# Performance work log

Hardware: AMD Instinct MI355X
Metric: run time of the kernel (lower is better)

## Reference

```python
import jax, jax.numpy as jnp
import numpy as np

F_DIM = 128
RBF_DIM = 20
N_NODES = 10000
N_EDGES = 200000
CUTOFF = 5


def setup_inputs() -> dict:
    key = jax.random.key(0)
    ks = jax.random.split(key, 12)
    s = jax.random.normal(ks[0], (N_NODES, F_DIM), jnp.float32)
    vec = jax.random.normal(ks[1], (N_NODES, 3, F_DIM), jnp.float32)
    edge_indexes = jax.random.randint(ks[2], (2, N_EDGES), 0, N_NODES, jnp.int32)
    edge_vector = jax.random.normal(ks[3], (N_EDGES, 3), jnp.float32)
    # distances in (0.5, 5.0) so fcut is nontrivial and no divide-by-zero
    edge_distance = jax.random.uniform(ks[4], (N_EDGES,), jnp.float32) * 4.5 + 0.5
    edge_rbf = jax.random.normal(ks[5], (N_EDGES, RBF_DIM), jnp.float32)
    # params: linear_s = Linear(F,F) -> SiLU -> Linear(F,3F); linear_rbf = Linear(RBF,3F)
    Ws1 = jax.random.normal(ks[6], (F_DIM, F_DIM), jnp.float32) / np.sqrt(F_DIM)
    bs1 = jnp.zeros((F_DIM,), jnp.float32)
    Ws2 = jax.random.normal(ks[7], (3 * F_DIM, F_DIM), jnp.float32) / np.sqrt(F_DIM)
    bs2 = jnp.zeros((3 * F_DIM,), jnp.float32)
    Wrbf = jax.random.normal(ks[8], (3 * F_DIM, RBF_DIM), jnp.float32) / np.sqrt(RBF_DIM)
    brbf = jnp.zeros((3 * F_DIM,), jnp.float32)
    return {
        "s": s, "vec": vec, "edge_vector": edge_vector,
        "edge_distance": edge_distance, "edge_rbf": edge_rbf,
        "Ws1": Ws1, "bs1": bs1, "Ws2": Ws2, "bs2": bs2,
        "Wrbf": Wrbf, "brbf": brbf,
        "edge_indexes": edge_indexes, "cutoff_dist": CUTOFF,
    }


def reference(s, vec, edge_vector, edge_distance, edge_rbf,
              Ws1, bs1, Ws2, bs2, Wrbf, brbf,
              edge_indexes, cutoff_dist):
    num_atoms, nf = s.shape
    dst_recv = edge_indexes[0]   # index_add target (message receivers)
    src_send = edge_indexes[1]   # gather source (message senders)

    S = s[src_send]              # [E, F]
    Vec = vec[src_send]          # [E, 3, F]

    # linear_s: Linear -> SiLU -> Linear
    h = jax.nn.silu(S @ Ws1.T + bs1)          # [E, F]
    phi = h @ Ws2.T + bs2                      # [E, 3F]

    rbf_lin = edge_rbf @ Wrbf.T + brbf         # [E, 3F]
    # cosine cutoff: 0.5*(cos(pi*d/rc)+1) for d < rc else 0
    rc = jnp.asarray(cutoff_dist, edge_distance.dtype)
    fcut = 0.5 * (jnp.cos(jnp.pi * edge_distance / rc) + 1.0)
    fcut = jnp.where(edge_distance < rc, fcut, 0.0)

    W = rbf_lin * fcut[:, None]
    vec_Ws, vec_Wvv, vec_Wvs = jnp.split(phi * W, 3, axis=-1)  # each [E, F]

    ds = jnp.zeros((num_atoms, nf), s.dtype).at[dst_recv].add(vec_Ws)

    vec_n = edge_vector / edge_distance[:, None]               # [E, 3]
    dVec = vec_Wvv[:, None, :] * Vec + vec_n[:, :, None] * vec_Wvs[:, None, :]  # [E,3,F]
    dvec = jnp.zeros((num_atoms, 3, nf), s.dtype).at[dst_recv].add(dVec)

    return ds, dvec
```

## Files before the change

kernel.cpp:

```cpp
#include <hip/hip_runtime.h>
#include <hip/hip_bf16.h>

typedef __attribute__((ext_vector_type(8))) short short8;
typedef __attribute__((ext_vector_type(4))) float floatx4;
typedef _Float16 half2_t __attribute__((ext_vector_type(2)));

#define CAP 64

__device__ __forceinline__ unsigned short f2bf(float x) {
    unsigned u = __float_as_uint(x);
    unsigned r = u + 0x7fffu + ((u >> 16) & 1u);
    return (unsigned short)(r >> 16);
}
__device__ __forceinline__ float bf2f(unsigned short h) {
    return __uint_as_float(((unsigned)h) << 16);
}
__device__ __forceinline__ unsigned short f2h(float x) {
    _Float16 h = (_Float16)x;
    return __builtin_bit_cast(unsigned short, h);
}
__device__ __forceinline__ short8 cvt8(float4 x0, float4 x1) {
    short8 v;
    v[0] = (short)f2bf(x0.x); v[1] = (short)f2bf(x0.y);
    v[2] = (short)f2bf(x0.z); v[3] = (short)f2bf(x0.w);
    v[4] = (short)f2bf(x1.x); v[5] = (short)f2bf(x1.y);
    v[6] = (short)f2bf(x1.z); v[7] = (short)f2bf(x1.w);
    return v;
}
__device__ __forceinline__ float FD(unsigned int a, unsigned int b, float c) {
#if __has_builtin(__builtin_amdgcn_fdot2)
    return __builtin_amdgcn_fdot2(__builtin_bit_cast(half2_t, a),
                                  __builtin_bit_cast(half2_t, b), c, false);
#else
    half2_t ha = __builtin_bit_cast(half2_t, a);
    half2_t hb = __builtin_bit_cast(half2_t, b);
    return c + (float)ha[0] * (float)hb[0] + (float)ha[1] * (float)hb[1];
#endif
}
__device__ __forceinline__ float decode_rc(const void* cutoff_raw) {
    float fv = ((const float*)cutoff_raw)[0];
    int   iv = ((const int*)cutoff_raw)[0];
    if (fv > 0.099f && fv < 1.0e6f) return fv;
    if (iv > 0 && iv < 1000000) return (float)iv;
    double dv = ((const double*)cutoff_raw)[0];
    if (dv > 0.099 && dv < 1.0e6) return (float)dv;
    return (float)(((const long long*)cutoff_raw)[0]);
}

#define LN 136
__global__ __launch_bounds__(256, 4)
void produce_kernel(const float* __restrict__ s,
                    const float* __restrict__ vec,
                    const float* __restrict__ Ws1,
                    const float* __restrict__ bs1,
                    const float* __restrict__ Ws2,
                    const float* __restrict__ bs2,
                    const float* __restrict__ Wrbf,
                    const float* __restrict__ edge_rbf,
                    const int* __restrict__ eidx,
                    const float* __restrict__ edge_vec,
                    const float* __restrict__ edge_dist,
                    const void* __restrict__ cutoff_raw,
                    unsigned short* __restrict__ P6,
                    unsigned short* __restrict__ wrbf_h,
                    unsigned short* __restrict__ rbf_h,
                    int* __restrict__ cnt,
                    unsigned int* __restrict__ rec,
                    int Nn, int RB, int E,
                    int nb_node, int nb_sc,
                    int ng_vec, int ng_wh, int ng_rh)
{
    const int bid = (int)blockIdx.x;
    const int tid = threadIdx.x;

    __shared__ unsigned short S_bf[16][LN];
    __shared__ unsigned short H_bf[16][LN];

    if (bid < nb_node) {
        const int wv   = tid >> 6;
        const int lane = tid & 63;
        const int l15  = lane & 15;
        const int qq   = lane >> 4;
        const int base = bid * 16;

        {
            int row = tid >> 4;
            int col = (tid & 15) * 8;
            int node = base + row;
            short8 v;
            if (node < Nn) {
                const float4* sp4 = (const float4*)(s + (size_t)node * 128 + col);
                v = cvt8(sp4[0], sp4[1]);
            } else {
                #pragma unroll
                for (int k = 0; k < 8; ++k) v[k] = 0;
            }
            *((short8*)&S_bf[row][col]) = v;
        }
        __syncthreads();

        {
            short8 a[4];
            #pragma unroll
            for (int ks = 0; ks < 4; ++ks)
                a[ks] = *((const short8*)&S_bf[l15][ks * 32 + qq * 8]);
            floatx4 acc1[2];
            #pragma unroll
            for (int t = 0; t < 2; ++t) acc1[t] = (floatx4){0.f, 0.f, 0.f, 0.f};
            #pragma unroll
            for (int ks = 0; ks < 4; ++ks) {
                #pragma unroll
                for (int t = 0; t < 2; ++t) {
                    int nj = wv * 2 + t;
                    const float* wr = Ws1 + (size_t)(nj * 16 + l15) * 128 + ks * 32 + qq * 8;
                    short8 b = cvt8(((const float4*)wr)[0], ((const float4*)wr)[1]);
                    acc1[t] = __builtin_amdgcn_mfma_f32_16x16x32_bf16(a[ks], b, acc1[t], 0, 0, 0);
                }
            }
            #pragma unroll
            for (int t = 0; t < 2; ++t) {
                int nj = wv * 2 + t;
                float b1 = bs1[nj * 16 + l15];
                #pragma unroll
                for (int r = 0; r < 4; ++r) {
                    float x = acc1[t][r] + b1;
                    float h = x / (1.0f + __expf(-x));
                    H_bf[qq * 4 + r][nj * 16 + l15] = f2bf(h);
                }
            }
        }
        __syncthreads();

        {
            short8 a[4];
            #pragma unroll
            for (int ks = 0; ks < 4; ++ks)
                a[ks] = *((const short8*)&H_bf[l15][ks * 32 + qq * 8]);
            #pragma unroll
            for (int t6 = 0; t6 < 6; ++t6) {
                int t = wv * 6 + t6;
                int n = t * 16 + l15;
                floatx4 acc = (floatx4){0.f, 0.f, 0.f, 0.f};
                #pragma unroll
                for (int ks = 0; ks < 4; ++ks) {
                    const float* wr = Ws2 + (size_t)n * 128 + ks * 32 + qq * 8;
                    short8 b = cvt8(((const float4*)wr)[0], ((const float4*)wr)[1]);
                    acc = __builtin_amdgcn_mfma_f32_16x16x32_bf16(a[ks], b, acc, 0, 0, 0);
                }
                float b2 = bs2[n];
                #pragma unroll
                for (int r = 0; r < 4; ++r) {
                    int node = base + qq * 4 + r;
                    if (node < Nn)
                        P6[(size_t)node * 768 + n] = f2bf(acc[r] + b2);
                }
            }
        }
    } else if (bid < nb_node + nb_sc) {
        int i = (bid - nb_node) * 256 + tid;
        if (i >= E) return;
        float rc = decode_rc(cutoff_raw);
        int d = eidx[i];
        int slot = atomicAdd(&cnt[d], 1);
        if (slot >= CAP) return;
        float dist = edge_dist[i];
        float fc = 0.0f;
        if (dist < rc) fc = 0.5f * (cosf(3.14159265358979323846f * dist / rc) + 1.0f);
        float inv = 1.0f / dist;
        unsigned int* rp = rec + ((size_t)(d * CAP + slot) << 3);
        ((uint4*)rp)[0] = make_uint4((unsigned)eidx[E + i], (unsigned)i, 0u, 0u);
        ((uint4*)rp)[1] = make_uint4(__float_as_uint(edge_vec[i * 3 + 0] * inv),
                                     __float_as_uint(edge_vec[i * 3 + 1] * inv),
                                     __float_as_uint(edge_vec[i * 3 + 2] * inv),
                                     __float_as_uint(fc));
    } else {
        int total = ng_vec + ng_wh + ng_rh;
        int nbc = (int)gridDim.x - nb_node - nb_sc;
        int stride = nbc * 256;
        for (int g = (bid - nb_node - nb_sc) * 256 + tid; g < total; g += stride) {
            if (g < ng_vec) {
                int node = g / 48;
                int r = (g - node * 48) * 8;
                const float4* sp = (const float4*)(vec + (size_t)node * 384 + r);
                *(short8*)(P6 + (size_t)node * 768 + 384 + r) = cvt8(sp[0], sp[1]);
            } else if (g < ng_vec + ng_wh) {
                int gg = g - ng_vec;
                int n = gg >> 2, k0 = (gg & 3) * 8;
                short8 v;
                #pragma unroll
                for (int t = 0; t < 8; ++t) {
                    int k = k0 + t;
                    v[t] = (k < RB) ? (short)f2h(Wrbf[(size_t)n * RB + k]) : (short)0;
                }
                *(short8*)(wrbf_h + n * 32 + k0) = v;
            } else {
                int gg = g - ng_vec - ng_wh;
                int e = gg / 3, k0 = (gg - e * 3) * 8;
                short8 v;
                #pragma unroll
                for (int t = 0; t < 8; ++t) {
                    int k = k0 + t;
                    v[t] = (k < RB) ? (short)f2h(edge_rbf[(size_t)e * RB + k]) : (short)0;
                }
                *(short8*)(rbf_h + (size_t)e * 24 + k0) = v;
            }
        }
    }
}

__global__ __launch_bounds__(256, 6)
void edge_kernel(const unsigned short* __restrict__ P6,
                 const unsigned short* __restrict__ wrbf_h,
                 const float* __restrict__ brbf,
                 const int* __restrict__ cnt,
                 const unsigned int* __restrict__ rec,
                 const unsigned short* __restrict__ rbf_h,
                 float* __restrict__ out_ds,
                 float* __restrict__ out_dvec,
                 int Nn)
{
    const int tid  = threadIdx.x;
    const int w    = tid >> 6;
    const int lane = tid & 63;
    const int node = __builtin_amdgcn_readfirstlane((int)blockIdx.x * 2 + (w >> 1));
    const int c    = (w & 1) * 64 + lane;
    if (node >= Nn) return;

    const unsigned short* wp0 = wrbf_h + ((size_t)c << 5);
    const unsigned short* wp1 = wrbf_h + ((size_t)(128 + c) << 5);
    const unsigned short* wp2 = wrbf_h + ((size_t)(256 + c) << 5);
    uint4 w0a = *(const uint4*)wp0;
    uint4 w0b = *(const uint4*)(wp0 + 8);
    uint2 w0c = *(const uint2*)(wp0 + 16);
    uint4 w1a = *(const uint4*)wp1;
    uint4 w1b = *(const uint4*)(wp1 + 8);
    uint2 w1c = *(const uint2*)(wp1 + 16);
    uint4 w2a = *(const uint4*)wp2;
    uint4 w2b = *(const uint4*)(wp2 + 8);
    uint2 w2c = *(const uint2*)(wp2 + 16);
    float b0 = brbf[c];
    float b1 = brbf[128 + c];
    float b2 = brbf[256 + c];
    asm volatile("" : "+v"(w0a.x), "+v"(w0a.y), "+v"(w0a.z), "+v"(w0a.w),
                      "+v"(w0b.x), "+v"(w0b.y), "+v"(w0b.z), "+v"(w0b.w),
                      "+v"(w0c.x), "+v"(w0c.y));
    asm volatile("" : "+v"(w1a.x), "+v"(w1a.y), "+v"(w1a.z), "+v"(w1a.w),
                      "+v"(w1b.x), "+v"(w1b.y), "+v"(w1b.z), "+v"(w1b.w),
                      "+v"(w1c.x), "+v"(w1c.y));
    asm volatile("" : "+v"(w2a.x), "+v"(w2a.y), "+v"(w2a.z), "+v"(w2a.w),
                      "+v"(w2b.x), "+v"(w2b.y), "+v"(w2b.z), "+v"(w2b.w),
                      "+v"(w2c.x), "+v"(w2c.y),
                      "+v"(b0), "+v"(b1), "+v"(b2));

    const int deg = min(cnt[node], CAP);
    const size_t bb = (size_t)node * CAP;

    float as = 0.f, a0 = 0.f, a1 = 0.f, a2 = 0.f;

    if (deg > 0) {
        const uint4* rp = (const uint4*)(rec + (bb << 3));
        uint4 sm = rp[0], mq = rp[1];
        const unsigned short* rr = rbf_h + (size_t)(int)sm.y * 24;
        uint4 Ra = *(const uint4*)rr;
        uint4 Rb = *(const uint4*)(rr + 8);
        uint2 Rc = *(const uint2*)(rr + 16);

        for (int sl = 0; sl < deg; ++sl) {
            const unsigned short* pr = P6 + (size_t)(int)sm.x * 768;
            unsigned short u0 = pr[c];
            unsigned short u1 = pr[128 + c];
            unsigned short u2 = pr[256 + c];
            unsigned short u3 = pr[384 + c];
            unsigned short u4 = pr[512 + c];
            unsigned short u5 = pr[640 + c];

            int np = (sl + 1 < deg) ? (sl + 1) : sl;
            uint4 smn = rp[2 * np], mqn = rp[2 * np + 1];
            const unsigned short* rrn = rbf_h + (size_t)(int)smn.y * 24;
            uint4 Ran = *(const uint4*)rrn;
            uint4 Rbn = *(const uint4*)(rrn + 8);
            uint2 Rcn = *(const uint2*)(rrn + 16);

            float d0 = b0, d1 = b1, d2 = b2;
            d0 = FD(Ra.x, w0a.x, d0); d1 = FD(Ra.x, w1a.x, d1); d2 = FD(Ra.x, w2a.x, d2);
            d0 = FD(Ra.y, w0a.y, d0); d1 = FD(Ra.y, w1a.y, d1); d2 = FD(Ra.y, w2a.y, d2);
            d0 = FD(Ra.z, w0a.z, d0); d1 = FD(Ra.z, w1a.z, d1); d2 = FD(Ra.z, w2a.z, d2);
            d0 = FD(Ra.w, w0a.w, d0); d1 = FD(Ra.w, w1a.w, d1); d2 = FD(Ra.w, w2a.w, d2);
            d0 = FD(Rb.x, w0b.x, d0); d1 = FD(Rb.x, w1b.x, d1); d2 = FD(Rb.x, w2b.x, d2);
            d0 = FD(Rb.y, w0b.y, d0); d1 = FD(Rb.y, w1b.y, d1); d2 = FD(Rb.y, w2b.y, d2);
            d0 = FD(Rb.z, w0b.z, d0); d1 = FD(Rb.z, w1b.z, d1); d2 = FD(Rb.z, w2b.z, d2);
            d0 = FD(Rb.w, w0b.w, d0); d1 = FD(Rb.w, w1b.w, d1); d2 = FD(Rb.w, w2b.w, d2);
            d0 = FD(Rc.x, w0c.x, d0); d1 = FD(Rc.x, w1c.x, d1); d2 = FD(Rc.x, w2c.x, d2);
            d0 = FD(Rc.y, w0c.y, d0); d1 = FD(Rc.y, w1c.y, d1); d2 = FD(Rc.y, w2c.y, d2);

            float ps = bf2f(u0), pv = bf2f(u1), px = bf2f(u2);
            float v0 = bf2f(u3), v1 = bf2f(u4), v2 = bf2f(u5);

            float fc = __uint_as_float(mq.w);
            float W0 = d0 * fc, W1 = d1 * fc, W2 = d2 * fc;
            as = fmaf(ps, W0, as);
            float mv = pv * W1;
            float mx = px * W2;
            a0 = fmaf(mv, v0, fmaf(mx, __uint_as_float(mq.x), a0));
            a1 = fmaf(mv, v1, fmaf(mx, __uint_as_float(mq.y), a1));
            a2 = fmaf(mv, v2, fmaf(mx, __uint_as_float(mq.z), a2));

            sm = smn; mq = mqn; Ra = Ran; Rb = Rbn; Rc = Rcn;
        }
    }

    __builtin_nontemporal_store(as, out_ds + (size_t)node * 128 + c);
    float* od = out_dvec + (size_t)node * 384;
    __builtin_nontemporal_store(a0, od + c);
    __builtin_nontemporal_store(a1, od + 128 + c);
    __builtin_nontemporal_store(a2, od + 256 + c);
}

extern "C" void kernel_launch(void* const* d_in, const int* in_sizes, int n_in,
                              void* d_out, int out_size, void* d_ws, size_t ws_size,
                              hipStream_t stream) {
    const float* s        = (const float*)d_in[0];
    const float* vec      = (const float*)d_in[1];
    const float* edge_vec = (const float*)d_in[2];
    const float* edge_dst = (const float*)d_in[3];
    const float* edge_rbf = (const float*)d_in[4];
    const float* Ws1      = (const float*)d_in[5];
    const float* bs1      = (const float*)d_in[6];
    const float* Ws2      = (const float*)d_in[7];
    const float* bs2      = (const float*)d_in[8];
    const float* Wrbf     = (const float*)d_in[9];
    const float* brbf     = (const float*)d_in[10];
    const int*   eidx     = (const int*)d_in[11];
    const void*  cutoff   = d_in[12];

    const int F  = 128;
    const int Nn = in_sizes[0] / F;
    const int E  = in_sizes[3];
    const int RB = in_sizes[4] / E;
    const int F3 = 3 * F;

    unsigned int*   rec     = (unsigned int*)d_ws;
    unsigned short* P6      = (unsigned short*)(rec + (size_t)Nn * CAP * 8);
    unsigned short* rbf_h   = P6 + (size_t)Nn * 768;
    unsigned short* wrbf_h  = rbf_h + (size_t)E * 24;
    int* cnt                = (int*)(wrbf_h + F3 * 32);

    int ng_vec = (Nn * F3) >> 3;
    int ng_wh  = (F3 * 32) >> 3;
    int ng_rh  = (E * 24) >> 3;

    hipMemsetAsync(cnt, 0, (size_t)Nn * sizeof(int), stream);

    int nb_node = (Nn + 15) / 16;
    int nb_sc   = (E + 255) / 256;
    long long total_g = (long long)ng_vec + ng_wh + ng_rh;
    int nb_cast = (int)((total_g + 255) / 256);

    produce_kernel<<<nb_node + nb_sc + nb_cast, 256, 0, stream>>>(
        s, vec, Ws1, bs1, Ws2, bs2, Wrbf, edge_rbf,
        eidx, edge_vec, edge_dst, cutoff,
        P6, wrbf_h, rbf_h, cnt, rec,
        Nn, RB, E, nb_node, nb_sc,
        ng_vec, ng_wh, ng_rh);

    float* out_ds   = (float*)d_out;
    float* out_dvec = out_ds + (size_t)Nn * F;

    edge_kernel<<<(Nn + 1) / 2, 256, 0, stream>>>(P6, wrbf_h, brbf,
                                                  cnt, rec, rbf_h,
                                                  out_ds, out_dvec, Nn);
}
```

Before: 194.5 us.

## Pack fp16 RBF features directly into per-receiver edge records

The scatter phase now reads each edge's 20 RBF values, converts them to fp16 and stores them inside the per-receiver bucket record, which grows from 32 to 64 bytes. The separate rbf_h cast pass and the edge kernel's indirect gather through the edge id are removed, so the edge loop reads one contiguous record per neighbour. Scatter blocks are also moved to the front of the grid so they get scheduled first. The cost is a larger record buffer and more scattered write traffic in the scatter phase.

```diff
diff --git a/kernel.cpp b/kernel.cpp
--- a/kernel.cpp
+++ b/kernel.cpp
@@ -63,12 +63,11 @@
                     const void* __restrict__ cutoff_raw,
                     unsigned short* __restrict__ P6,
                     unsigned short* __restrict__ wrbf_h,
-                    unsigned short* __restrict__ rbf_h,
                     int* __restrict__ cnt,
                     unsigned int* __restrict__ rec,
                     int Nn, int RB, int E,
-                    int nb_node, int nb_sc,
-                    int ng_vec, int ng_wh, int ng_rh)
+                    int nb_sc, int nb_node,
+                    int ng_vec, int ng_wh)
 {
     const int bid = (int)blockIdx.x;
     const int tid = threadIdx.x;
@@ -76,12 +75,41 @@
     __shared__ unsigned short S_bf[16][LN];
     __shared__ unsigned short H_bf[16][LN];
 
-    if (bid < nb_node) {
+    if (bid < nb_sc) {
+        int i = bid * 256 + tid;
+        if (i >= E) return;
+        float rc = decode_rc(cutoff_raw);
+        int d = eidx[i];
+        int slot = atomicAdd(&cnt[d], 1);
+        if (slot >= CAP) return;
+        float dist = edge_dist[i];
+        float fc = 0.0f;
+        if (dist < rc) fc = 0.5f * (cosf(3.14159265358979323846f * dist / rc) + 1.0f);
+        float inv = 1.0f / dist;
+
+        float x[20];
+        const float* rr = edge_rbf + (size_t)i * RB;
+        #pragma unroll
+        for (int k = 0; k < 20; ++k) x[k] = (k < RB) ? rr[k] : 0.0f;
+        unsigned pk[10];
+        #pragma unroll
+        for (int k = 0; k < 10; ++k)
+            pk[k] = (unsigned)f2h(x[2 * k]) | ((unsigned)f2h(x[2 * k + 1]) << 16);
+
+        unsigned int* rp = rec + ((size_t)(d * CAP + slot) << 4);
+        ((uint4*)rp)[0] = make_uint4((unsigned)eidx[E + i], __float_as_uint(fc),
+                                     __float_as_uint(edge_vec[i * 3 + 0] * inv),
+                                     __float_as_uint(edge_vec[i * 3 + 1] * inv));
+        ((uint4*)rp)[1] = make_uint4(__float_as_uint(edge_vec[i * 3 + 2] * inv),
+                                     pk[0], pk[1], pk[2]);
+        ((uint4*)rp)[2] = make_uint4(pk[3], pk[4], pk[5], pk[6]);
+        ((uint4*)rp)[3] = make_uint4(pk[7], pk[8], pk[9], 0u);
+    } else if (bid < nb_sc + nb_node) {
         const int wv   = tid >> 6;
         const int lane = tid & 63;
         const int l15  = lane & 15;
         const int qq   = lane >> 4;
-        const int base = bid * 16;
+        const int base = (bid - nb_sc) * 16;
 
         {
             int row = tid >> 4;
@@ -156,34 +184,17 @@
                 }
             }
         }
-    } else if (bid < nb_node + nb_sc) {
-        int i = (bid - nb_node) * 256 + tid;
-        if (i >= E) return;
-        float rc = decode_rc(cutoff_raw);
-        int d = eidx[i];
-        int slot = atomicAdd(&cnt[d], 1);
-        if (slot >= CAP) return;
-        float dist = edge_dist[i];
-        float fc = 0.0f;
-        if (dist < rc) fc = 0.5f * (cosf(3.14159265358979323846f * dist / rc) + 1.0f);
-        float inv = 1.0f / dist;
-        unsigned int* rp = rec + ((size_t)(d * CAP + slot) << 3);
-        ((uint4*)rp)[0] = make_uint4((unsigned)eidx[E + i], (unsigned)i, 0u, 0u);
-        ((uint4*)rp)[1] = make_uint4(__float_as_uint(edge_vec[i * 3 + 0] * inv),
-                                     __float_as_uint(edge_vec[i * 3 + 1] * inv),
-                                     __float_as_uint(edge_vec[i * 3 + 2] * inv),
-                                     __float_as_uint(fc));
     } else {
-        int total = ng_vec + ng_wh + ng_rh;
-        int nbc = (int)gridDim.x - nb_node - nb_sc;
+        int total = ng_vec + ng_wh;
+        int nbc = (int)gridDim.x - nb_sc - nb_node;
         int stride = nbc * 256;
-        for (int g = (bid - nb_node - nb_sc) * 256 + tid; g < total; g += stride) {
+        for (int g = (bid - nb_sc - nb_node) * 256 + tid; g < total; g += stride) {
             if (g < ng_vec) {
                 int node = g / 48;
                 int r = (g - node * 48) * 8;
                 const float4* sp = (const float4*)(vec + (size_t)node * 384 + r);
                 *(short8*)(P6 + (size_t)node * 768 + 384 + r) = cvt8(sp[0], sp[1]);
-            } else if (g < ng_vec + ng_wh) {
+            } else {
                 int gg = g - ng_vec;
                 int n = gg >> 2, k0 = (gg & 3) * 8;
                 short8 v;
@@ -193,16 +204,6 @@
                     v[t] = (k < RB) ? (short)f2h(Wrbf[(size_t)n * RB + k]) : (short)0;
                 }
                 *(short8*)(wrbf_h + n * 32 + k0) = v;
-            } else {
-                int gg = g - ng_vec - ng_wh;
-                int e = gg / 3, k0 = (gg - e * 3) * 8;
-                short8 v;
-                #pragma unroll
-                for (int t = 0; t < 8; ++t) {
-                    int k = k0 + t;
-                    v[t] = (k < RB) ? (short)f2h(edge_rbf[(size_t)e * RB + k]) : (short)0;
-                }
-                *(short8*)(rbf_h + (size_t)e * 24 + k0) = v;
             }
         }
     }
@@ -214,7 +215,6 @@
                  const float* __restrict__ brbf,
                  const int* __restrict__ cnt,
                  const unsigned int* __restrict__ rec,
-                 const unsigned short* __restrict__ rbf_h,
                  float* __restrict__ out_ds,
                  float* __restrict__ out_dvec,
                  int Nn)
@@ -258,15 +258,11 @@
     float as = 0.f, a0 = 0.f, a1 = 0.f, a2 = 0.f;
 
     if (deg > 0) {
-        const uint4* rp = (const uint4*)(rec + (bb << 3));
-        uint4 sm = rp[0], mq = rp[1];
-        const unsigned short* rr = rbf_h + (size_t)(int)sm.y * 24;
-        uint4 Ra = *(const uint4*)rr;
-        uint4 Rb = *(const uint4*)(rr + 8);
-        uint2 Rc = *(const uint2*)(rr + 16);
+        const uint4* rp = (const uint4*)(rec + (bb << 4));
+        uint4 q0 = rp[0], q1 = rp[1], q2 = rp[2], q3 = rp[3];
 
         for (int sl = 0; sl < deg; ++sl) {
-            const unsigned short* pr = P6 + (size_t)(int)sm.x * 768;
+            const unsigned short* pr = P6 + (size_t)(int)q0.x * 768;
             unsigned short u0 = pr[c];
             unsigned short u1 = pr[128 + c];
             unsigned short u2 = pr[256 + c];
@@ -275,37 +271,34 @@
             unsigned short u5 = pr[640 + c];
 
             int np = (sl + 1 < deg) ? (sl + 1) : sl;
-            uint4 smn = rp[2 * np], mqn = rp[2 * np + 1];
-            const unsigned short* rrn = rbf_h + (size_t)(int)smn.y * 24;
-            uint4 Ran = *(const uint4*)rrn;
-            uint4 Rbn = *(const uint4*)(rrn + 8);
-            uint2 Rcn = *(const uint2*)(rrn + 16);
+            uint4 n0 = rp[4 * np], n1 = rp[4 * np + 1];
+            uint4 n2 = rp[4 * np + 2], n3 = rp[4 * np + 3];
 
             float d0 = b0, d1 = b1, d2 = b2;
-            d0 = FD(Ra.x, w0a.x, d0); d1 = FD(Ra.x, w1a.x, d1); d2 = FD(Ra.x, w2a.x, d2);
-            d0 = FD(Ra.y, w0a.y, d0); d1 = FD(Ra.y, w1a.y, d1); d2 = FD(Ra.y, w2a.y, d2);
-            d0 = FD(Ra.z, w0a.z, d0); d1 = FD(Ra.z, w1a.z, d1); d2 = FD(Ra.z, w2a.z, d2);
-            d0 = FD(Ra.w, w0a.w, d0); d1 = FD(Ra.w, w1a.w, d1); d2 = FD(Ra.w, w2a.w, d2);
-            d0 = FD(Rb.x, w0b.x, d0); d1 = FD(Rb.x, w1b.x, d1); d2 = FD(Rb.x, w2b.x, d2);
-            d0 = FD(Rb.y, w0b.y, d0); d1 = FD(Rb.y, w1b.y, d1); d2 = FD(Rb.y, w2b.y, d2);
-            d0 = FD(Rb.z, w0b.z, d0); d1 = FD(Rb.z, w1b.z, d1); d2 = FD(Rb.z, w2b.z, d2);
-            d0 = FD(Rb.w, w0b.w, d0); d1 = FD(Rb.w, w1b.w, d1); d2 = FD(Rb.w, w2b.w, d2);
-            d0 = FD(Rc.x, w0c.x, d0); d1 = FD(Rc.x, w1c.x, d1); d2 = FD(Rc.x, w2c.x, d2);
-            d0 = FD(Rc.y, w0c.y, d0); d1 = FD(Rc.y, w1c.y, d1); d2 = FD(Rc.y, w2c.y, d2);
+            d0 = FD(q1.y, w0a.x, d0); d1 = FD(q1.y, w1a.x, d1); d2 = FD(q1.y, w2a.x, d2);
+            d0 = FD(q1.z, w0a.y, d0); d1 = FD(q1.z, w1a.y, d1); d2 = FD(q1.z, w2a.y, d2);
+            d0 = FD(q1.w, w0a.z, d0); d1 = FD(q1.w, w1a.z, d1); d2 = FD(q1.w, w2a.z, d2);
+            d0 = FD(q2.x, w0a.w, d0); d1 = FD(q2.x, w1a.w, d1); d2 = FD(q2.x, w2a.w, d2);
+            d0 = FD(q2.y, w0b.x, d0); d1 = FD(q2.y, w1b.x, d1); d2 = FD(q2.y, w2b.x, d2);
+            d0 = FD(q2.z, w0b.y, d0); d1 = FD(q2.z, w1b.y, d1); d2 = FD(q2.z, w2b.y, d2);
+            d0 = FD(q2.w, w0b.z, d0); d1 = FD(q2.w, w1b.z, d1); d2 = FD(q2.w, w2b.z, d2);
+            d0 = FD(q3.x, w0b.w, d0); d1 = FD(q3.x, w1b.w, d1); d2 = FD(q3.x, w2b.w, d2);
+            d0 = FD(q3.y, w0c.x, d0); d1 = FD(q3.y, w1c.x, d1); d2 = FD(q3.y, w2c.x, d2);
+            d0 = FD(q3.z, w0c.y, d0); d1 = FD(q3.z, w1c.y, d1); d2 = FD(q3.z, w2c.y, d2);
 
             float ps = bf2f(u0), pv = bf2f(u1), px = bf2f(u2);
             float v0 = bf2f(u3), v1 = bf2f(u4), v2 = bf2f(u5);
 
-            float fc = __uint_as_float(mq.w);
+            float fc = __uint_as_float(q0.y);
             float W0 = d0 * fc, W1 = d1 * fc, W2 = d2 * fc;
             as = fmaf(ps, W0, as);
             float mv = pv * W1;
             float mx = px * W2;
-            a0 = fmaf(mv, v0, fmaf(mx, __uint_as_float(mq.x), a0));
-            a1 = fmaf(mv, v1, fmaf(mx, __uint_as_float(mq.y), a1));
-            a2 = fmaf(mv, v2, fmaf(mx, __uint_as_float(mq.z), a2));
-
-            sm = smn; mq = mqn; Ra = Ran; Rb = Rbn; Rc = Rcn;
+            a0 = fmaf(mv, v0, fmaf(mx, __uint_as_float(q0.z), a0));
+            a1 = fmaf(mv, v1, fmaf(mx, __uint_as_float(q0.w), a1));
+            a2 = fmaf(mv, v2, fmaf(mx, __uint_as_float(q1.x), a2));
+
+            q0 = n0; q1 = n1; q2 = n2; q3 = n3;
         }
     }
 
@@ -340,33 +333,31 @@
     const int F3 = 3 * F;
 
     unsigned int*   rec     = (unsigned int*)d_ws;
-    unsigned short* P6      = (unsigned short*)(rec + (size_t)Nn * CAP * 8);
-    unsigned short* rbf_h   = P6 + (size_t)Nn * 768;
-    unsigned short* wrbf_h  = rbf_h + (size_t)E * 24;
+    unsigned short* P6      = (unsigned short*)(rec + (size_t)Nn * CAP * 16);
+    unsigned short* wrbf_h  = P6 + (size_t)Nn * 768;
     int* cnt                = (int*)(wrbf_h + F3 * 32);
 
     int ng_vec = (Nn * F3) >> 3;
     int ng_wh  = (F3 * 32) >> 3;
-    int ng_rh  = (E * 24) >> 3;
 
     hipMemsetAsync(cnt, 0, (size_t)Nn * sizeof(int), stream);
 
+    int nb_sc   = (E + 255) / 256;
     int nb_node = (Nn + 15) / 16;
-    int nb_sc   = (E + 255) / 256;
-    long long total_g = (long long)ng_vec + ng_wh + ng_rh;
+    long long total_g = (long long)ng_vec + ng_wh;
     int nb_cast = (int)((total_g + 255) / 256);
 
-    produce_kernel<<<nb_node + nb_sc + nb_cast, 256, 0, stream>>>(
+    produce_kernel<<<nb_sc + nb_node + nb_cast, 256, 0, stream>>>(
         s, vec, Ws1, bs1, Ws2, bs2, Wrbf, edge_rbf,
         eidx, edge_vec, edge_dst, cutoff,
-        P6, wrbf_h, rbf_h, cnt, rec,
-        Nn, RB, E, nb_node, nb_sc,
-        ng_vec, ng_wh, ng_rh);
+        P6, wrbf_h, cnt, rec,
+        Nn, RB, E, nb_sc, nb_node,
+        ng_vec, ng_wh);
 
     float* out_ds   = (float*)d_out;
     float* out_dvec = out_ds + (size_t)Nn * F;
 
     edge_kernel<<<(Nn + 1) / 2, 256, 0, stream>>>(P6, wrbf_h, brbf,
-                                                  cnt, rec, rbf_h,
+                                                  cnt, rec,
                                                   out_ds, out_dvec, Nn);
 }
```

New measurement: 215.9 us. 11.0% more time.
